# Kernel tuning notes

Measured on AMD Instinct MI355X. Metric: run time of the kernel, lower is better.

## Reference

```python
import jax, jax.numpy as jnp
import numpy as np

N, IN, HID, OUT, E, G = 20000, 256, 256, 128, 320000, 64


def setup_inputs() -> dict:
    key = jax.random.key(0)
    ks = jax.random.split(key, 16)
    s = 0.05
    x = jax.random.normal(ks[0], (N, IN), jnp.float32)
    edge_index = jax.random.randint(ks[1], (2, E), 0, N, dtype=jnp.int32)
    batch = jnp.sort(jax.random.randint(ks[2], (N,), 0, G, dtype=jnp.int32))
    return {
        "x": x,
        "edge_index": edge_index,
        "batch": batch,
        "num_graphs": G,
        "W1": jax.random.normal(ks[3], (HID, IN), jnp.float32) * s,
        "b1": jnp.zeros((HID,), jnp.float32),
        "W2": jax.random.normal(ks[4], (HID, HID), jnp.float32) * s,
        "b2": jnp.zeros((HID,), jnp.float32),
        "W3": jax.random.normal(ks[5], (HID, HID), jnp.float32) * s,
        "b3": jnp.zeros((HID,), jnp.float32),
        "W4": jax.random.normal(ks[6], (OUT, HID), jnp.float32) * s,
        "b4": jnp.zeros((OUT,), jnp.float32),
        "lin_w": jax.random.normal(ks[7], (1, OUT), jnp.float32) * s,
        "lin_b": jnp.zeros((1,), jnp.float32),
    }


def reference(x, edge_index, batch, num_graphs, W1, b1, W2, b2, W3, b3, W4, b4, lin_w, lin_b):
    row, col = edge_index[0], edge_index[1]
    n = x.shape[0]
    # degree-based symmetric-ish norm (as in source: degree of row only)
    deg = jax.ops.segment_sum(jnp.ones((row.shape[0],), x.dtype), row, num_segments=n)
    deg_inv_sqrt = deg ** -0.5  # 0-degree -> inf, matching torch deg.pow(-0.5)
    norm = (deg_inv_sqrt[row] * deg_inv_sqrt[col])[:, None]  # [E,1]

    def gcn_layer(h, W, b):
        h = h @ W.T + b                                  # dense linear [N,out]
        msgs = norm * h[row]                             # gather + scale [E,out]
        return jax.ops.segment_sum(msgs, col, num_segments=n)  # scatter-add

    h = gcn_layer(x, W1, b1)
    h = gcn_layer(h, W2, b2)
    h = gcn_layer(h, W3, b3)
    h = gcn_layer(h, W4, b4)

    # to_dense_batch(...).mean(dim=1): sum per graph / max graph size (padded mean)
    sums = jax.ops.segment_sum(h, batch, num_segments=num_graphs)          # [G,OUT]
    counts = jax.ops.segment_sum(jnp.ones((n,), h.dtype), batch, num_segments=num_graphs)
    x_new = sums / jnp.max(counts)
    return x_new @ lin_w.T + lin_b  # [G,1]
```

## Files before the change

### kernel.cpp

```cpp
#include <hip/hip_runtime.h>
#include <math.h>

#define NN      20000
#define IN_DIM  256
#define HID_DIM 256
#define OUT_DIM 128
#define EE      320000
#define GG      64

#define P_H     8
#define CHUNK   (EE / P_H)
#define NW      10000
#define PSTRIDE 10240
#define CHB     16
#define MGB     20
#define SB      1250
#define GB      313


__device__ __forceinline__ float ldf_mall(const float* p) {
  return __hip_atomic_load(p, __ATOMIC_RELAXED, __HIP_MEMORY_SCOPE_AGENT);
}
__device__ __forceinline__ int ldi_mall(const int* p) {
  return __hip_atomic_load(p, __ATOMIC_RELAXED, __HIP_MEMORY_SCOPE_AGENT);
}

__global__ __launch_bounds__(1024) void k_hist_chain(
    const int* __restrict__ erow, const int* __restrict__ ecol,
    unsigned int* __restrict__ pdeg, unsigned int* __restrict__ pccnt,
    unsigned short* __restrict__ rankb,
    const float* __restrict__ W1, const float* __restrict__ b1,
    const float* __restrict__ W2, const float* __restrict__ b2,
    const float* __restrict__ W3, const float* __restrict__ b3,
    const float* __restrict__ W4, const float* __restrict__ b4,
    const float* __restrict__ lw,
    float* __restrict__ q4g, float* __restrict__ q3g,
    float* __restrict__ q2g, float* __restrict__ q1g,
    float* __restrict__ dv, int* __restrict__ chaindone) {
  __shared__ __align__(16) char smem[40960];
  const int bid = blockIdx.x, tid = threadIdx.x;

  if (bid < 2 * P_H) {
    unsigned int* h = (unsigned int*)smem;
    const int  p   = bid & (P_H - 1);
    const bool isc = bid >= P_H;
    const int* src = isc ? ecol : erow;
    unsigned int* slab = (isc ? pccnt : pdeg) + (size_t)p * PSTRIDE;
    for (int w = tid; w < NW; w += 1024) h[w] = 0u;
    __syncthreads();
    const int base = p * CHUNK;
    for (int i = tid; i < CHUNK; i += 1024) {
      int v = src[base + i];
      int sh = (v & 1) << 4;
      unsigned int old = atomicAdd(&h[v >> 1], 1u << sh);
      if (isc) rankb[base + i] = (unsigned short)((old >> sh) & 0xFFFFu);
    }
    __syncthreads();
    for (int w = tid; w < NW; w += 1024) slab[w] = h[w];
    return;
  }

  const int cb = bid - 2 * P_H;
  float* fs  = (float*)smem;
  float* lwl = fs;
  float* qs4 = fs + 128;
  float* qs3 = fs + 384;
  float* qs2 = fs + 640;
  float* part = fs + 896;
  float* red  = fs + 1920;
  const int jj = tid & 15, tt = tid >> 4;
  const int jg = cb * 16 + jj;

  if (tid < 128) lwl[tid] = lw[tid];
  __syncthreads();

  auto arrive_wait = [&](int target) {
    __syncthreads();
    if (tid == 0) {
      __hip_atomic_fetch_add(chaindone, 1, __ATOMIC_RELEASE, __HIP_MEMORY_SCOPE_AGENT);
      while (__hip_atomic_load(chaindone, __ATOMIC_RELAXED, __HIP_MEMORY_SCOPE_AGENT) < target)
        __builtin_amdgcn_s_sleep(1);
      (void)__hip_atomic_load(chaindone, __ATOMIC_ACQUIRE, __HIP_MEMORY_SCOPE_AGENT);
    }
    __syncthreads();
  };
  auto stage = [&](const float* W, const float* qin, int K, float* qout_g) {
    float acc = 0.f;
    for (int t = tt; t < K; t += 64) acc += W[(size_t)t * 256 + jg] * qin[t];
    part[tt * 16 + jj] = acc;
    __syncthreads();
    if (tid < 16) {
      float s = 0.f;
#pragma unroll
      for (int k = 0; k < 64; ++k) s += part[k * 16 + tid];
      qout_g[cb * 16 + tid] = s;
    }
  };
  auto load_q = [&](const float* qg, float* qdst) {
    if (tid < 256) qdst[tid] = ldf_mall(qg + tid);
    __syncthreads();
  };

  stage(W4, lwl, OUT_DIM, q4g);  arrive_wait(1 * CHB);
  load_q(q4g, qs4);
  stage(W3, qs4, HID_DIM, q3g);  arrive_wait(2 * CHB);
  load_q(q3g, qs3);
  stage(W2, qs3, HID_DIM, q2g);  arrive_wait(3 * CHB);
  load_q(q2g, qs2);
  stage(W1, qs2, HID_DIM, q1g);

  if (cb == 0) {
    __syncthreads();
    auto dot = [&](const float* a, const float* bl, int K, float* dst) {
      float p = (tid < K) ? a[tid] * bl[tid] : 0.f;
#pragma unroll
      for (int off = 32; off; off >>= 1) p += __shfl_down(p, off);
      if ((tid & 63) == 0) red[tid >> 6] = p;
      __syncthreads();
      if (tid == 0) { float s = 0.f; for (int k = 0; k < 16; ++k) s += red[k]; *dst = s; }
      __syncthreads();
    };
    dot(b1, qs2, HID_DIM, &dv[0]);
    dot(b2, qs3, HID_DIM, &dv[1]);
    dot(b3, qs4, HID_DIM, &dv[2]);
    dot(b4, lwl, OUT_DIM, &dv[3]);
  }
}

__global__ __launch_bounds__(1024) void k_msc_mv(
    const unsigned int* __restrict__ pdeg, const unsigned int* __restrict__ pccnt,
    int* __restrict__ deg, int* __restrict__ ccnt,
    unsigned short* __restrict__ chunkoff, int* __restrict__ mergedone,
    int* __restrict__ cstart,
    const int* __restrict__ batch, float* __restrict__ outcnt,
    const float* __restrict__ x, const float* __restrict__ q1,
    float* __restrict__ u0) {
  int bid = blockIdx.x, tid = threadIdx.x, lane = tid & 63, wid = tid >> 6;

  if (bid == 0) {
    if (tid == 0) {
      while (__hip_atomic_load(mergedone, __ATOMIC_RELAXED, __HIP_MEMORY_SCOPE_AGENT) < MGB)
        __builtin_amdgcn_s_sleep(1);
      (void)__hip_atomic_load(mergedone, __ATOMIC_ACQUIRE, __HIP_MEMORY_SCOPE_AGENT);
    }
    __syncthreads();
    __shared__ int ws[16];
    const int PER = 20;
    int base = tid * PER;
    int v[PER]; int sum = 0;
#pragma unroll
    for (int i = 0; i < PER; ++i) {
      int idx = base + i;
      v[i] = (idx < NN) ? ldi_mall(&ccnt[idx]) : 0;
      sum += v[i];
    }
    int incl = sum;
#pragma unroll
    for (int off = 1; off < 64; off <<= 1) { int t = __shfl_up(incl, off); if (lane >= off) incl += t; }
    if (lane == 63) ws[wid] = incl;
    __syncthreads();
    if (tid == 0) { int r = 0; for (int j = 0; j < 16; ++j) { int t = ws[j]; ws[j] = r; r += t; } }
    __syncthreads();
    int run = ws[wid] + incl - sum;
#pragma unroll
    for (int i = 0; i < PER; ++i) {
      int idx = base + i;
      if (idx < NN) cstart[idx] = run;
      run += v[i];
    }
    if (tid == 1023) cstart[NN] = run;
    return;
  }

  if (bid <= MGB) {
    int w0 = (bid - 1) * 500;
    for (int w = w0 + tid; w < w0 + 500; w += 1024) {
      unsigned int dlo = 0, dhi = 0, clo = 0, chi = 0;
      const int c0 = 2 * w, c1 = 2 * w + 1;
#pragma unroll
      for (int p = 0; p < P_H; ++p) {
        unsigned int ud = pdeg[(size_t)p * PSTRIDE + w];
        unsigned int uc = pccnt[(size_t)p * PSTRIDE + w];
        dlo += ud & 0xFFFFu; dhi += ud >> 16;
        chunkoff[(size_t)c0 * P_H + p] = (unsigned short)clo;
        chunkoff[(size_t)c1 * P_H + p] = (unsigned short)chi;
        clo += uc & 0xFFFFu; chi += uc >> 16;
      }
      deg[c0]  = (int)dlo; deg[c1]  = (int)dhi;
      ccnt[c0] = (int)clo; ccnt[c1] = (int)chi;
    }
    __syncthreads();
    if (tid == 0)
      __hip_atomic_fetch_add(mergedone, 1, __ATOMIC_RELEASE, __HIP_MEMORY_SCOPE_AGENT);
    return;
  }

  if (bid == MGB + 1) {
    for (int base = 0; base < NN; base += 1024) {
      int n = base + tid;
      int b = -1; float cn = 0.f;
      if (n < NN) { b = batch[n]; cn = 1.f; }
#pragma unroll
      for (int off = 1; off < 64; off <<= 1) {
        float c2 = __shfl_up(cn, off);
        int   b2 = __shfl_up(b, off);
        if (lane >= off && b2 == b) cn += c2;
      }
      int bn = __shfl_down(b, 1);
      if (((lane == 63) || (bn != b)) && b >= 0) atomicAdd(&outcnt[b], cn);
    }
    return;
  }

  int r = (bid - (MGB + 2)) * 16 + wid;
  if (r >= NN) return;
  const float4 xv = *(const float4*)(x + (size_t)r * IN_DIM + lane * 4);
  const float4 qv = *(const float4*)(q1 + lane * 4);
  float s = xv.x * qv.x + xv.y * qv.y + xv.z * qv.z + xv.w * qv.w;
#pragma unroll
  for (int off = 32; off; off >>= 1) s += __shfl_down(s, off);
  if (lane == 0) u0[r] = s;
}

__global__ __launch_bounds__(256) void k_scatter(
    const int* __restrict__ erow, const int* __restrict__ ecol,
    const int* __restrict__ deg, const int* __restrict__ cstart,
    const unsigned short* __restrict__ chunkoff,
    const unsigned short* __restrict__ rankb,
    int2* __restrict__ sedge) {
  int e = blockIdx.x * 256 + threadIdx.x;
  int r = erow[e], c = ecol[e];
  int p = e / CHUNK;
  int slot = cstart[c] + (int)chunkoff[(size_t)c * P_H + p] + (int)rankb[e];
  float dr = (float)deg[r], dc = (float)deg[c];
  float val = (1.0f / sqrtf(dr)) * (1.0f / sqrtf(dc));
  sedge[slot] = make_int2(r, __float_as_int(val));
}

__global__ __launch_bounds__(256) void k_gather(
    const int* __restrict__ cstart, const int2* __restrict__ sedge,
    const float* __restrict__ uin, const float* __restrict__ dptr,
    float* __restrict__ uout) {
  int gid = blockIdx.x * 256 + threadIdx.x;
  int n = gid >> 2, l = gid & 3;
  if (n >= NN) return;
  int s0 = cstart[n], s1 = cstart[n + 1];
  float acc = 0.f, es = 0.f;
  for (int s = s0 + l; s < s1; s += 4) {
    int2 ev = sedge[s];
    float v = __int_as_float(ev.y);
    acc += v * uin[ev.x];
    es  += v;
  }
  acc += __shfl_xor(acc, 1); es += __shfl_xor(es, 1);
  acc += __shfl_xor(acc, 2); es += __shfl_xor(es, 2);
  if (l == 0) uout[n] = acc + dptr[0] * es;
}

__global__ __launch_bounds__(256) void k_gather_pool_final(
    const int* __restrict__ cstart, const int2* __restrict__ sedge,
    const float* __restrict__ uin, const float* __restrict__ dptr,
    const int* __restrict__ batch, float* __restrict__ outsum,
    const float* __restrict__ outcnt, const float* __restrict__ lb,
    float* __restrict__ out, int* __restrict__ done, int nblocks) {
  int gid = blockIdx.x * 256 + threadIdx.x;
  int lane = threadIdx.x & 63;
  int n = gid >> 2, l = gid & 3;
  float pv = 0.f; int b = -1;
  if (n < NN) {
    int s0 = cstart[n], s1 = cstart[n + 1];
    float acc = 0.f, es = 0.f;
    for (int s = s0 + l; s < s1; s += 4) {
      int2 ev = sedge[s];
      float v = __int_as_float(ev.y);
      acc += v * uin[ev.x];
      es  += v;
    }
    acc += __shfl_xor(acc, 1); es += __shfl_xor(es, 1);
    acc += __shfl_xor(acc, 2); es += __shfl_xor(es, 2);
    b = batch[n];
    if (l == 0) pv = acc + dptr[0] * es;
  }
#pragma unroll
  for (int off = 1; off < 64; off <<= 1) {
    float s2 = __shfl_up(pv, off);
    int   b2 = __shfl_up(b, off);
    if (lane >= off && b2 == b) pv += s2;
  }
  int bn = __shfl_down(b, 1);
  if (((lane == 63) || (bn != b)) && b >= 0) atomicAdd(&outsum[b], pv);

  __syncthreads();
  __shared__ int winner;
  if (threadIdx.x == 0) {
    int old = __hip_atomic_fetch_add(done, 1, __ATOMIC_RELAXED, __HIP_MEMORY_SCOPE_AGENT);
    winner = (old == nblocks - 1) ? 1 : 0;
  }
  __syncthreads();
  if (winner && threadIdx.x < GG) {
    int g = threadIdx.x;
    float m = ldf_mall(&outcnt[g]);
#pragma unroll
    for (int off = 32; off; off >>= 1) m = fmaxf(m, __shfl_xor(m, off));
    out[g] = ldf_mall(&outsum[g]) / m + lb[0];
  }
}

extern "C" void kernel_launch(void* const* d_in, const int* in_sizes, int n_in,
                              void* d_out, int out_size, void* d_ws, size_t ws_size,
                              hipStream_t stream) {
  (void)in_sizes; (void)n_in; (void)out_size; (void)ws_size;
  const float* x     = (const float*)d_in[0];
  const int*   erow  = (const int*)d_in[1];
  const int*   ecol  = ((const int*)d_in[1]) + EE;
  const int*   batch = (const int*)d_in[2];
  const float* W1 = (const float*)d_in[4];
  const float* b1 = (const float*)d_in[5];
  const float* W2 = (const float*)d_in[6];
  const float* b2 = (const float*)d_in[7];
  const float* W3 = (const float*)d_in[8];
  const float* b3 = (const float*)d_in[9];
  const float* W4 = (const float*)d_in[10];
  const float* b4 = (const float*)d_in[11];
  const float* lw = (const float*)d_in[12];
  const float* lb = (const float*)d_in[13];
  float* out = (float*)d_out;

  const size_t PN = 80128;
  char* w = (char*)d_ws;
  float* outsum    = (float*)w;  w += 256;
  float* outcnt    = (float*)w;  w += 256;
  int*   done      = (int*)w;    w += 256;
  int*   mergedone = (int*)w;    w += 256;
  int*   chaindone = (int*)w;    w += 256;
  size_t zbytes = (size_t)(w - (char*)d_ws);
  int*   deg    = (int*)w;    w += PN;
  int*   ccnt   = (int*)w;    w += PN;
  int*   cstart = (int*)w;    w += PN + 256;
  int2*  sedge  = (int2*)w;   w += (size_t)EE * 8;
  unsigned int*   pdeg  = (unsigned int*)w;   w += (size_t)P_H * PSTRIDE * 4;
  unsigned int*   pccnt = (unsigned int*)w;   w += (size_t)P_H * PSTRIDE * 4;
  unsigned short* chunkoff = (unsigned short*)w; w += (size_t)NN * P_H * 2;
  unsigned short* rankb    = (unsigned short*)w; w += (size_t)EE * 2;
  float* q4 = (float*)w;  w += 1024;
  float* q3 = (float*)w;  w += 1024;
  float* q2 = (float*)w;  w += 1024;
  float* q1 = (float*)w;  w += 1024;
  float* dv = (float*)w;  w += 256;
  float* u0 = (float*)w;  w += PN;
  float* u1 = (float*)w;  w += PN;
  float* u2 = (float*)w;  w += PN;
  float* u3 = (float*)w;  w += PN;

  hipMemsetAsync(d_ws, 0, zbytes, stream);
  k_hist_chain<<<2 * P_H + CHB, 1024, 0, stream>>>(erow, ecol, pdeg, pccnt, rankb,
                                                   W1, b1, W2, b2, W3, b3, W4, b4,
                                                   lw, q4, q3, q2, q1, dv, chaindone);
  k_msc_mv<<<MGB + 2 + 1250, 1024, 0, stream>>>(pdeg, pccnt, deg, ccnt, chunkoff,
                                                mergedone, cstart, batch, outcnt,
                                                x, q1, u0);
  k_scatter<<<SB, 256, 0, stream>>>(erow, ecol, deg, cstart, chunkoff, rankb, sedge);
  k_gather<<<GB, 256, 0, stream>>>(cstart, sedge, u0, dv + 0, u1);
  k_gather<<<GB, 256, 0, stream>>>(cstart, sedge, u1, dv + 1, u2);
  k_gather<<<GB, 256, 0, stream>>>(cstart, sedge, u2, dv + 2, u3);
  k_gather_pool_final<<<GB, 256, 0, stream>>>(cstart, sedge, u3, dv + 3, batch,
                                              outsum, outcnt, lb, out, done, GB);
}
```

Baseline: 82.41 us.

## Replace cross-block weight chain with per-block GEMVs, fuse scatter into merge kernel

Each chain block now computes the full W4→W3→W2→W1 matrix-vector chain redundantly in shared memory, which removes the grid-wide arrive/wait barriers and the global q4/q3/q2 buffers. The hipMemsetAsync is dropped; block 0 of the histogram kernel zeroes the counter region itself. The edge scatter kernel is merged into the merge/scan/matvec kernel as extra blocks that spin on a scan-done flag, saving one launch. In exchange the weight chain does redundant global reads in every block, and the spinning scatter blocks can occupy compute units while they wait for the scan block.

New measurement: 82.85 us (median of 2 runs). About the same (+0.5%).

```diff
diff --git a/kernel.cpp b/kernel.cpp
--- a/kernel.cpp
+++ b/kernel.cpp
@@ -14,7 +14,8 @@
 #define PSTRIDE 10240
 #define CHB     16
 #define MGB     20
-#define SB      1250
+#define MVB     1250
+#define SCB2    313
 #define GB      313
 
 
@@ -28,19 +29,18 @@
 __global__ __launch_bounds__(1024) void k_hist_chain(
     const int* __restrict__ erow, const int* __restrict__ ecol,
     unsigned int* __restrict__ pdeg, unsigned int* __restrict__ pccnt,
-    unsigned short* __restrict__ rankb,
+    unsigned short* __restrict__ rankb, int* __restrict__ zctr,
     const float* __restrict__ W1, const float* __restrict__ b1,
     const float* __restrict__ W2, const float* __restrict__ b2,
     const float* __restrict__ W3, const float* __restrict__ b3,
     const float* __restrict__ W4, const float* __restrict__ b4,
-    const float* __restrict__ lw,
-    float* __restrict__ q4g, float* __restrict__ q3g,
-    float* __restrict__ q2g, float* __restrict__ q1g,
-    float* __restrict__ dv, int* __restrict__ chaindone) {
+    const float* __restrict__ lw, float* __restrict__ q1g,
+    float* __restrict__ dv) {
   __shared__ __align__(16) char smem[40960];
   const int bid = blockIdx.x, tid = threadIdx.x;
 
   if (bid < 2 * P_H) {
+    if (bid == 0 && tid < 320) zctr[tid] = 0;
     unsigned int* h = (unsigned int*)smem;
     const int  p   = bid & (P_H - 1);
     const bool isc = bid >= P_H;
@@ -62,55 +62,39 @@
 
   const int cb = bid - 2 * P_H;
   float* fs  = (float*)smem;
-  float* lwl = fs;
-  float* qs4 = fs + 128;
-  float* qs3 = fs + 384;
-  float* qs2 = fs + 640;
-  float* part = fs + 896;
-  float* red  = fs + 1920;
-  const int jj = tid & 15, tt = tid >> 4;
-  const int jg = cb * 16 + jj;
-
-  if (tid < 128) lwl[tid] = lw[tid];
+  float* lws = fs;
+  float* qa  = fs + 128;
+  float* qb  = fs + 384;
+  float* qc  = fs + 640;
+  float* qd  = fs + 896;
+  float* part = fs + 1152;
+  float* red  = fs + 2176;
+  const int j = tid & 255, tq = tid >> 8;
+
+  if (tid < 128) lws[tid] = lw[tid];
   __syncthreads();
 
-  auto arrive_wait = [&](int target) {
-    __syncthreads();
-    if (tid == 0) {
-      __hip_atomic_fetch_add(chaindone, 1, __ATOMIC_RELEASE, __HIP_MEMORY_SCOPE_AGENT);
-      while (__hip_atomic_load(chaindone, __ATOMIC_RELAXED, __HIP_MEMORY_SCOPE_AGENT) < target)
-        __builtin_amdgcn_s_sleep(1);
-      (void)__hip_atomic_load(chaindone, __ATOMIC_ACQUIRE, __HIP_MEMORY_SCOPE_AGENT);
-    }
+  auto gemv = [&](const float* W, const float* qin, float* qout, int K) {
+    const int quarter = K >> 2, t0 = tq * quarter;
+    float s = 0.f;
+#pragma unroll 4
+    for (int m = 0; m < quarter; ++m) {
+      int t = t0 + m;
+      s += W[(size_t)t * 256 + j] * qin[t];
+    }
+    part[tq * 256 + j] = s;
+    __syncthreads();
+    if (tq == 0) qout[j] = part[j] + part[256 + j] + part[512 + j] + part[768 + j];
     __syncthreads();
   };
-  auto stage = [&](const float* W, const float* qin, int K, float* qout_g) {
-    float acc = 0.f;
-    for (int t = tt; t < K; t += 64) acc += W[(size_t)t * 256 + jg] * qin[t];
-    part[tt * 16 + jj] = acc;
-    __syncthreads();
-    if (tid < 16) {
-      float s = 0.f;
-#pragma unroll
-      for (int k = 0; k < 64; ++k) s += part[k * 16 + tid];
-      qout_g[cb * 16 + tid] = s;
-    }
-  };
-  auto load_q = [&](const float* qg, float* qdst) {
-    if (tid < 256) qdst[tid] = ldf_mall(qg + tid);
-    __syncthreads();
-  };
-
-  stage(W4, lwl, OUT_DIM, q4g);  arrive_wait(1 * CHB);
-  load_q(q4g, qs4);
-  stage(W3, qs4, HID_DIM, q3g);  arrive_wait(2 * CHB);
-  load_q(q3g, qs3);
-  stage(W2, qs3, HID_DIM, q2g);  arrive_wait(3 * CHB);
-  load_q(q2g, qs2);
-  stage(W1, qs2, HID_DIM, q1g);
+
+  gemv(W4, lws, qa, OUT_DIM);
+  gemv(W3, qa, qb, HID_DIM);
+  gemv(W2, qb, qc, HID_DIM);
+  gemv(W1, qc, qd, HID_DIM);
+  if (tid < 16) q1g[cb * 16 + tid] = qd[cb * 16 + tid];
 
   if (cb == 0) {
-    __syncthreads();
     auto dot = [&](const float* a, const float* bl, int K, float* dst) {
       float p = (tid < K) ? a[tid] * bl[tid] : 0.f;
 #pragma unroll
@@ -120,21 +104,23 @@
       if (tid == 0) { float s = 0.f; for (int k = 0; k < 16; ++k) s += red[k]; *dst = s; }
       __syncthreads();
     };
-    dot(b1, qs2, HID_DIM, &dv[0]);
-    dot(b2, qs3, HID_DIM, &dv[1]);
-    dot(b3, qs4, HID_DIM, &dv[2]);
-    dot(b4, lwl, OUT_DIM, &dv[3]);
-  }
-}
-
-__global__ __launch_bounds__(1024) void k_msc_mv(
+    dot(b1, qc, HID_DIM, &dv[0]);
+    dot(b2, qb, HID_DIM, &dv[1]);
+    dot(b3, qa, HID_DIM, &dv[2]);
+    dot(b4, lws, OUT_DIM, &dv[3]);
+  }
+}
+
+__global__ __launch_bounds__(1024) void k_mssc_mv(
     const unsigned int* __restrict__ pdeg, const unsigned int* __restrict__ pccnt,
     int* __restrict__ deg, int* __restrict__ ccnt,
     unsigned short* __restrict__ chunkoff, int* __restrict__ mergedone,
-    int* __restrict__ cstart,
+    int* __restrict__ scandone, int* __restrict__ cstart,
     const int* __restrict__ batch, float* __restrict__ outcnt,
     const float* __restrict__ x, const float* __restrict__ q1,
-    float* __restrict__ u0) {
+    float* __restrict__ u0,
+    const int* __restrict__ erow, const int* __restrict__ ecol,
+    const unsigned short* __restrict__ rankb, int2* __restrict__ sedge) {
   int bid = blockIdx.x, tid = threadIdx.x, lane = tid & 63, wid = tid >> 6;
 
   if (bid == 0) {
@@ -159,7 +145,7 @@
     for (int off = 1; off < 64; off <<= 1) { int t = __shfl_up(incl, off); if (lane >= off) incl += t; }
     if (lane == 63) ws[wid] = incl;
     __syncthreads();
-    if (tid == 0) { int r = 0; for (int j = 0; j < 16; ++j) { int t = ws[j]; ws[j] = r; r += t; } }
+    if (tid == 0) { int r = 0; for (int k = 0; k < 16; ++k) { int t = ws[k]; ws[k] = r; r += t; } }
     __syncthreads();
     int run = ws[wid] + incl - sum;
 #pragma unroll
@@ -169,6 +155,9 @@
       run += v[i];
     }
     if (tid == 1023) cstart[NN] = run;
+    __syncthreads();
+    if (tid == 0)
+      __hip_atomic_fetch_add(scandone, 1, __ATOMIC_RELEASE, __HIP_MEMORY_SCOPE_AGENT);
     return;
   }
 
@@ -212,23 +201,26 @@
     return;
   }
 
-  int r = (bid - (MGB + 2)) * 16 + wid;
-  if (r >= NN) return;
-  const float4 xv = *(const float4*)(x + (size_t)r * IN_DIM + lane * 4);
-  const float4 qv = *(const float4*)(q1 + lane * 4);
-  float s = xv.x * qv.x + xv.y * qv.y + xv.z * qv.z + xv.w * qv.w;
-#pragma unroll
-  for (int off = 32; off; off >>= 1) s += __shfl_down(s, off);
-  if (lane == 0) u0[r] = s;
-}
-
-__global__ __launch_bounds__(256) void k_scatter(
-    const int* __restrict__ erow, const int* __restrict__ ecol,
-    const int* __restrict__ deg, const int* __restrict__ cstart,
-    const unsigned short* __restrict__ chunkoff,
-    const unsigned short* __restrict__ rankb,
-    int2* __restrict__ sedge) {
-  int e = blockIdx.x * 256 + threadIdx.x;
+  if (bid < MGB + 2 + MVB) {
+    int r = (bid - (MGB + 2)) * 16 + wid;
+    if (r >= NN) return;
+    const float4 xv = *(const float4*)(x + (size_t)r * IN_DIM + lane * 4);
+    const float4 qv = *(const float4*)(q1 + lane * 4);
+    float s = xv.x * qv.x + xv.y * qv.y + xv.z * qv.z + xv.w * qv.w;
+#pragma unroll
+    for (int off = 32; off; off >>= 1) s += __shfl_down(s, off);
+    if (lane == 0) u0[r] = s;
+    return;
+  }
+
+  if (tid == 0) {
+    while (__hip_atomic_load(scandone, __ATOMIC_RELAXED, __HIP_MEMORY_SCOPE_AGENT) < 1)
+      __builtin_amdgcn_s_sleep(1);
+    (void)__hip_atomic_load(scandone, __ATOMIC_ACQUIRE, __HIP_MEMORY_SCOPE_AGENT);
+  }
+  __syncthreads();
+  int e = (bid - (MGB + 2 + MVB)) * 1024 + tid;
+  if (e >= EE) return;
   int r = erow[e], c = ecol[e];
   int p = e / CHUNK;
   int slot = cstart[c] + (int)chunkoff[(size_t)c * P_H + p] + (int)rankb[e];
@@ -332,8 +324,7 @@
   float* outcnt    = (float*)w;  w += 256;
   int*   done      = (int*)w;    w += 256;
   int*   mergedone = (int*)w;    w += 256;
-  int*   chaindone = (int*)w;    w += 256;
-  size_t zbytes = (size_t)(w - (char*)d_ws);
+  int*   scandone  = (int*)w;    w += 256;
   int*   deg    = (int*)w;    w += PN;
   int*   ccnt   = (int*)w;    w += PN;
   int*   cstart = (int*)w;    w += PN + 256;
@@ -342,9 +333,6 @@
   unsigned int*   pccnt = (unsigned int*)w;   w += (size_t)P_H * PSTRIDE * 4;
   unsigned short* chunkoff = (unsigned short*)w; w += (size_t)NN * P_H * 2;
   unsigned short* rankb    = (unsigned short*)w; w += (size_t)EE * 2;
-  float* q4 = (float*)w;  w += 1024;
-  float* q3 = (float*)w;  w += 1024;
-  float* q2 = (float*)w;  w += 1024;
   float* q1 = (float*)w;  w += 1024;
   float* dv = (float*)w;  w += 256;
   float* u0 = (float*)w;  w += PN;
@@ -352,14 +340,13 @@
   float* u2 = (float*)w;  w += PN;
   float* u3 = (float*)w;  w += PN;
 
-  hipMemsetAsync(d_ws, 0, zbytes, stream);
-  k_hist_chain<<<2 * P_H + CHB, 1024, 0, stream>>>(erow, ecol, pdeg, pccnt, rankb,
+  k_hist_chain<<<2 * P_H + CHB, 1024, 0, stream>>>(erow, ecol, pdeg, pccnt,
+                                                   rankb, (int*)d_ws,
                                                    W1, b1, W2, b2, W3, b3, W4, b4,
-                                                   lw, q4, q3, q2, q1, dv, chaindone);
-  k_msc_mv<<<MGB + 2 + 1250, 1024, 0, stream>>>(pdeg, pccnt, deg, ccnt, chunkoff,
-                                                mergedone, cstart, batch, outcnt,
-                                                x, q1, u0);
-  k_scatter<<<SB, 256, 0, stream>>>(erow, ecol, deg, cstart, chunkoff, rankb, sedge);
+                                                   lw, q1, dv);
+  k_mssc_mv<<<MGB + 2 + MVB + SCB2, 1024, 0, stream>>>(
+      pdeg, pccnt, deg, ccnt, chunkoff, mergedone, scandone, cstart,
+      batch, outcnt, x, q1, u0, erow, ecol, rankb, sedge);
   k_gather<<<GB, 256, 0, stream>>>(cstart, sedge, u0, dv + 0, u1);
   k_gather<<<GB, 256, 0, stream>>>(cstart, sedge, u1, dv + 1, u2);
   k_gather<<<GB, 256, 0, stream>>>(cstart, sedge, u2, dv + 2, u3);
```
